# Performance work log

Hardware: AMD Instinct MI355X
Metric: run time of the kernel (lower is better)

Reference implementation:

```python
import jax, jax.numpy as jnp
import numpy as np
from jax import lax

WINDOW = (3, 7, 7)   # per-axis neighborhood kernel size (odd -> centered window)
TILE = (4, 8, 8)     # query tile per axis (must divide T,H,W); FNA-style tiling


def _axis_window(X, k, tq):
    # NATTEN non-causal, stride=1, dilation=1: query i attends keys [s, s+k)
    # with s = clip(i - (k-1)//2, 0, X-k) (centered, clamped at borders).
    starts = np.clip(np.arange(X) - (k - 1) // 2, 0, X - k)          # [X]
    span = tq + k - 1                                                # key block extent per tile
    lead = np.arange(X // tq) * tq                                   # first query of each tile
    base = np.minimum(starts[lead], X - span)                        # [nt] block start (in-bounds)
    gq = lead[:, None] + np.arange(tq)                                # [nt, tq] global query idx
    s = starts[gq][..., None]                                        # [nt, tq, 1]
    j = base[:, None, None] + np.arange(span)                         # [nt, 1, span] global key idx
    valid = (j >= s) & (j < s + k)                                    # [nt, tq, span]
    return base.astype(np.int32), valid


def _na3d(q, k, v, T, H, W):
    B, L, nh, D = q.shape
    assert L == T * H * W
    kT, kH, kW = WINDOW
    qt, qh, qw = TILE
    assert T % qt == 0 and H % qh == 0 and W % qw == 0
    st, sh, sw = qt + kT - 1, qh + kH - 1, qw + kW - 1
    ntT, ntH, ntW = T // qt, H // qh, W // qw
    N = ntT * ntH * ntW
    qvol, svol = qt * qh * qw, st * sh * sw

    baseT, mT = _axis_window(T, kT, qt)
    baseH, mH = _axis_window(H, kH, qh)
    baseW, mW = _axis_window(W, kW, qw)

    # combined per-tile mask: [N, qvol, svol] (static, small)
    mask = (mT[:, None, None, :, None, None, :, None, None]
            & mH[None, :, None, None, :, None, None, :, None]
            & mW[None, None, :, None, None, :, None, None, :])
    mask = jnp.asarray(mask.reshape(N, qvol, svol))

    bT, bH, bW = np.meshgrid(baseT, baseH, baseW, indexing='ij')
    bT = jnp.asarray(bT.ravel()); bH = jnp.asarray(bH.ravel()); bW = jnp.asarray(bW.ravel())

    def to_grid(x):
        return x.reshape(B, T, H, W, nh, D)
    qg, kg, vg = to_grid(q), to_grid(k), to_grid(v)

    # query tiles -> [N, B, qvol, nh, D]
    qt_ = qg.reshape(B, ntT, qt, ntH, qh, ntW, qw, nh, D)
    qt_ = qt_.transpose(1, 3, 5, 0, 2, 4, 6, 7, 8).reshape(N, B, qvol, nh, D)

    # key/value halo blocks per tile -> [N, B, svol, nh, D]
    def slice_blk(arr, t0, h0, w0):
        return lax.dynamic_slice(arr, (0, t0, h0, w0, 0, 0), (B, st, sh, sw, nh, D))
    kblk = jax.vmap(slice_blk, in_axes=(None, 0, 0, 0))(kg, bT, bH, bW).reshape(N, B, svol, nh, D)
    vblk = jax.vmap(slice_blk, in_axes=(None, 0, 0, 0))(vg, bT, bH, bW).reshape(N, B, svol, nh, D)

    scale = D ** -0.5
    scores = jnp.einsum('nbqhd,nbkhd->nbhqk', qt_, kblk) * scale
    scores = jnp.where(mask[:, None, None], scores, -jnp.inf)
    attn = jax.nn.softmax(scores, axis=-1)
    out = jnp.einsum('nbhqk,nbkhd->nbhqd', attn, vblk)

    # scatter tiles back to [B, L, nh, D]
    out = out.reshape(ntT, ntH, ntW, B, nh, qt, qh, qw, D)
    out = out.transpose(3, 0, 5, 1, 6, 2, 7, 4, 8).reshape(B, L, nh, D)
    return out


def setup_inputs() -> dict:
    key = jax.random.key(0)
    k1, k2, k3 = jax.random.split(key, 3)
    B, nh, D = 1, 8, 128
    T, H, W = 16, 32, 32
    L = T * H * W
    q = jax.random.normal(k1, (B, L, nh, D), jnp.float32)
    kk = jax.random.normal(k2, (B, L, nh, D), jnp.float32)
    v = jax.random.normal(k3, (B, L, nh, D), jnp.float32)
    return {"q": q, "k": kk, "v": v, "video_t": T, "video_h": H, "video_w": W}


def reference(q, k, v, video_t, video_h, video_w):
    return _na3d(q, k, v, video_t, video_h, video_w)
```

## Files before the change

kernel.cpp:

```cpp
#include <hip/hip_runtime.h>


typedef _Float16 f16;
typedef _Float16 half8 __attribute__((ext_vector_type(8)));
typedef float floatx4 __attribute__((ext_vector_type(4)));

namespace {

constexpr int T = 16, H = 32, W = 32, NH = 8, D = 128;
constexpr int QT = 2, QH = 4, QW = 8;
constexpr float SCALE = 0.088388347648318447f;

__device__ __forceinline__ int SLOT(int tile, int lr) {
  return tile * 69 + (lr >> 4) * 17 + (lr & 15);
}

__device__ __forceinline__ size_t goff(int tt, int hh, int ww, int head) {
  return ((size_t)((tt * H + hh) * W + ww) * NH + head) * D;
}

__global__ __launch_bounds__(256) void na3d_mfma(
    const float* __restrict__ qp, const float* __restrict__ kp,
    const float* __restrict__ vp, float* __restrict__ op) {
  __shared__ alignas(16) f16 qbuf[16 * 69 * 8];
  __shared__ alignas(16) f16 kvbuf[24 * 69 * 8];
  __shared__ alignas(16) float st[80 * 65];
  __shared__ alignas(16) f16 pbuf[12 * 69 * 8];
  __shared__ alignas(16) float red[4 * 64];
  __shared__ alignas(16) float mnew[64];
  __shared__ alignas(16) float alphas[64];

  int bid = blockIdx.x;
  const int wb = bid & 3;  bid >>= 2;
  const int hb = bid & 7;  bid >>= 3;
  const int tb = bid & 7;  bid >>= 3;
  const int head = bid;

  const int t0 = tb * QT;
  const int h0 = hb * QH, w0 = wb * QW;
  const int bT = min(max(t0 - 1, 0), T - 4);
  const int bH = min(max(h0 - 3, 0), H - 10);
  const int bW = min(max(w0 - 3, 0), W - 14);

  const int tid = threadIdx.x;
  const int wave = tid >> 6, lane = tid & 63;
  const int quad = lane >> 4, ln = lane & 15;

  for (int s = tid; s < 1024; s += 256) {
    const int q = s >> 4, dg = s & 15;
    const size_t off =
        goff(t0 + (q >> 5), h0 + ((q >> 3) & 3), w0 + (q & 7), head) + dg * 8;
    const float4 x0 = *(const float4*)(qp + off);
    const float4 x1 = *(const float4*)(qp + off + 4);
    half8 hv;
    hv[0] = (f16)(x0.x * SCALE); hv[1] = (f16)(x0.y * SCALE);
    hv[2] = (f16)(x0.z * SCALE); hv[3] = (f16)(x0.w * SCALE);
    hv[4] = (f16)(x1.x * SCALE); hv[5] = (f16)(x1.y * SCALE);
    hv[6] = (f16)(x1.z * SCALE); hv[7] = (f16)(x1.w * SCALE);
    const int mt = q >> 4, m = q & 15, ks = dg >> 2, qd = dg & 3;
    *(half8*)&qbuf[SLOT(mt * 4 + ks, qd * 16 + m) * 8] = hv;
  }

  floatx4 oacc[8] = {{0.f, 0.f, 0.f, 0.f}, {0.f, 0.f, 0.f, 0.f},
                     {0.f, 0.f, 0.f, 0.f}, {0.f, 0.f, 0.f, 0.f},
                     {0.f, 0.f, 0.f, 0.f}, {0.f, 0.f, 0.f, 0.f},
                     {0.f, 0.f, 0.f, 0.f}, {0.f, 0.f, 0.f, 0.f}};

  float m_run = -1e30f, l_run = 0.f;

  const int sq = tid & 63, sp = tid >> 6;
  const int aT = min(max(t0 + (sq >> 5) - 1, 0), T - 3) - bT;
  const int aH = min(max(h0 + ((sq >> 3) & 3) - 3, 0), H - 7) - bH;
  const int aW = min(max(w0 + (sq & 7) - 3, 0), W - 7) - bW;

  for (int c = 0; c < 8; ++c) {
    const int dt = c >> 1, hh = c & 1;
    const int tt = bT + dt;
    const int kh0 = bH + hh * 5;
    const bool tOK = (dt >= aT) && (dt < aT + 3);

    __syncthreads();
    for (int s = tid; s < 1120; s += 256) {
      const int kk = s >> 4, dg = s & 15;
      const int khl = kk / 14, kw = kk - khl * 14;
      const size_t off = goff(tt, kh0 + khl, bW + kw, head) + dg * 8;
      const float4 x0 = *(const float4*)(kp + off);
      const float4 x1 = *(const float4*)(kp + off + 4);
      half8 hv;
      hv[0] = (f16)x0.x; hv[1] = (f16)x0.y; hv[2] = (f16)x0.z; hv[3] = (f16)x0.w;
      hv[4] = (f16)x1.x; hv[5] = (f16)x1.y; hv[6] = (f16)x1.z; hv[7] = (f16)x1.w;
      const int nt = kk >> 4, n = kk & 15, ks = dg >> 2, qd = dg & 3;
      *(half8*)&kvbuf[SLOT(nt * 4 + ks, qd * 16 + n) * 8] = hv;
    }
    __syncthreads();

    for (int tile = wave; tile < 20; tile += 4) {
      const int mt = tile / 5, nt = tile - mt * 5;
      floatx4 acc = {0.f, 0.f, 0.f, 0.f};
#pragma unroll
      for (int ks = 0; ks < 4; ++ks) {
        const half8 a = *(const half8*)&qbuf[SLOT(mt * 4 + ks, lane) * 8];
        const half8 b = *(const half8*)&kvbuf[SLOT(nt * 4 + ks, lane) * 8];
        acc = __builtin_amdgcn_mfma_f32_16x16x32_f16(a, b, acc, 0, 0, 0);
      }
      float* dst = &st[(nt * 16 + ln) * 65 + mt * 16 + quad * 4];
      dst[0] = acc[0]; dst[1] = acc[1]; dst[2] = acc[2]; dst[3] = acc[3];
    }
    __syncthreads();

    float pm = -1e30f;
    if (tOK) {
#pragma unroll
      for (int i = 0; i < 18; ++i) {
        const int kk = sp * 18 + i;
        if (kk < 70) {
          const int khl = kk / 14, kw = kk - khl * 14;
          const int kha = hh * 5 + khl;
          if (kha >= aH && kha < aH + 7 && kw >= aW && kw < aW + 7)
            pm = fmaxf(pm, st[kk * 65 + sq]);
        }
      }
    }
    red[sp * 64 + sq] = pm;
    __syncthreads();
    if (tid < 64) {
      float mc = red[tid];
#pragma unroll
      for (int p = 1; p < 4; ++p) mc = fmaxf(mc, red[p * 64 + tid]);
      const float mN = fmaxf(m_run, mc);
      const float a = __expf(m_run - mN);
      m_run = mN; l_run *= a;
      mnew[tid] = mN; alphas[tid] = a;
    }
    __syncthreads();

    {
      const float mq = mnew[sq];
      float ps = 0.f;
      const int mt = sq >> 4, m = sq & 15;
#pragma unroll
      for (int g = 0; g < 3; ++g) {
        const int b = sp * 3 + g;
        const int kst = b >> 2, qd = b & 3;
        half8 pv8;
#pragma unroll
        for (int j = 0; j < 8; ++j) {
          const int kk = b * 8 + j;
          float e = 0.f;
          if (tOK && kk < 70) {
            const int khl = kk / 14, kw = kk - khl * 14;
            const int kha = hh * 5 + khl;
            if (kha >= aH && kha < aH + 7 && kw >= aW && kw < aW + 7) {
              e = __expf(st[kk * 65 + sq] - mq);
              ps += e;
            }
          }
          pv8[j] = (f16)e;
        }
        *(half8*)&pbuf[SLOT(mt * 3 + kst, qd * 16 + m) * 8] = pv8;
      }
      red[sp * 64 + sq] = ps;
    }

    for (int s = tid; s < 1536; s += 256) {
      const int kk = s >> 4, dg = s & 15;
      float xs[8] = {0.f, 0.f, 0.f, 0.f, 0.f, 0.f, 0.f, 0.f};
      if (kk < 70) {
        const int khl = kk / 14, kw = kk - khl * 14;
        const size_t off = goff(tt, kh0 + khl, bW + kw, head) + dg * 8;
        const float4 x0 = *(const float4*)(vp + off);
        const float4 x1 = *(const float4*)(vp + off + 4);
        xs[0] = x0.x; xs[1] = x0.y; xs[2] = x0.z; xs[3] = x0.w;
        xs[4] = x1.x; xs[5] = x1.y; xs[6] = x1.z; xs[7] = x1.w;
      }
      const int kst = kk >> 5, qd = (kk >> 3) & 3, j = kk & 7;
      const int d0 = dg * 8;
#pragma unroll
      for (int u = 0; u < 8; ++u) {
        const int d = d0 + u;
        kvbuf[SLOT((d >> 4) * 3 + kst, qd * 16 + (d & 15)) * 8 + j] =
            (f16)xs[u];
      }
    }
    __syncthreads();

    if (tid < 64) {
      float s2 = 0.f;
#pragma unroll
      for (int p = 0; p < 4; ++p) s2 += red[p * 64 + tid];
      l_run += s2;
    }

    const floatx4 af = *(const floatx4*)&alphas[wave * 16 + quad * 4];
#pragma unroll
    for (int u = 0; u < 8; ++u) oacc[u] *= af;
#pragma unroll
    for (int ks = 0; ks < 3; ++ks) {
      const half8 a = *(const half8*)&pbuf[SLOT(wave * 3 + ks, lane) * 8];
#pragma unroll
      for (int u = 0; u < 8; ++u) {
        const half8 b = *(const half8*)&kvbuf[SLOT(u * 3 + ks, lane) * 8];
        oacc[u] = __builtin_amdgcn_mfma_f32_16x16x32_f16(a, b, oacc[u], 0, 0, 0);
      }
    }
  }

  __syncthreads();
  if (tid < 64) mnew[tid] = 1.f / l_run;
  __syncthreads();
  const floatx4 lf = *(const floatx4*)&mnew[wave * 16 + quad * 4];
#pragma unroll
  for (int r = 0; r < 4; ++r) {
    const int q = wave * 16 + quad * 4 + r;
    const size_t off =
        goff(t0 + (q >> 5), h0 + ((q >> 3) & 3), w0 + (q & 7), head);
#pragma unroll
    for (int u = 0; u < 8; ++u)
      op[off + u * 16 + ln] = oacc[u][r] * lf[r];
  }
}

}

extern "C" void kernel_launch(void* const* d_in, const int* in_sizes, int n_in,
                              void* d_out, int out_size, void* d_ws,
                              size_t ws_size, hipStream_t stream) {
  const float* q = (const float*)d_in[0];
  const float* k = (const float*)d_in[1];
  const float* v = (const float*)d_in[2];
  float* out = (float*)d_out;
  const int nblocks = NH * (T / QT) * (H / QH) * (W / QW);
  na3d_mfma<<<dim3(nblocks), dim3(256), 0, stream>>>(q, k, v, out);
}
```

Before: 528.5 us.

## Keep Q in registers, compute S^T per wave, prefetch K, softmax via shuffles

The kernel now holds the scaled Q fragments in registers and computes the transposed score tile per wave with MFMA. Each wave's 16 queries stay in its accumulators, so the shared-memory score buffer, the reduction arrays and several block barriers go away, and the running max and sum are reduced with cross-lane shuffles. K for the next chunk is prefetched into registers during softmax, and V loads are issued early, with pairs of key rows packed as half2 into shared memory. Custom barriers, a cheaper divide-by-14 and a launch bound of 3 blocks per CU are also added. The cost is much higher register pressure, which may force spills, and more complex indexing.

```diff
diff --git a/kernel.cpp b/kernel.cpp
--- a/kernel.cpp
+++ b/kernel.cpp
@@ -3,7 +3,15 @@
 
 typedef _Float16 f16;
 typedef _Float16 half8 __attribute__((ext_vector_type(8)));
+typedef _Float16 half4 __attribute__((ext_vector_type(4)));
+typedef _Float16 half2 __attribute__((ext_vector_type(2)));
 typedef float floatx4 __attribute__((ext_vector_type(4)));
+typedef float floatv4 __attribute__((ext_vector_type(4)));
+
+#define CFENCE() asm volatile("" ::: "memory")
+#define BAR_PLAIN() do { CFENCE(); __builtin_amdgcn_s_barrier(); CFENCE(); } while (0)
+#define BAR_LDSW() do { asm volatile("s_waitcnt lgkmcnt(0)" ::: "memory"); \
+                        __builtin_amdgcn_s_barrier(); CFENCE(); } while (0)
 
 namespace {
 
@@ -19,16 +27,13 @@
   return ((size_t)((tt * H + hh) * W + ww) * NH + head) * D;
 }
 
-__global__ __launch_bounds__(256) void na3d_mfma(
+__device__ __forceinline__ int div14(int x) { return (x * 586) >> 13; }
+
+__global__ __launch_bounds__(256, 3) void na3d_mfma(
     const float* __restrict__ qp, const float* __restrict__ kp,
     const float* __restrict__ vp, float* __restrict__ op) {
-  __shared__ alignas(16) f16 qbuf[16 * 69 * 8];
   __shared__ alignas(16) f16 kvbuf[24 * 69 * 8];
-  __shared__ alignas(16) float st[80 * 65];
   __shared__ alignas(16) f16 pbuf[12 * 69 * 8];
-  __shared__ alignas(16) float red[4 * 64];
-  __shared__ alignas(16) float mnew[64];
-  __shared__ alignas(16) float alphas[64];
 
   int bid = blockIdx.x;
   const int wb = bid & 3;  bid >>= 2;
@@ -45,153 +50,201 @@
   const int tid = threadIdx.x;
   const int wave = tid >> 6, lane = tid & 63;
   const int quad = lane >> 4, ln = lane & 15;
-
-  for (int s = tid; s < 1024; s += 256) {
-    const int q = s >> 4, dg = s & 15;
-    const size_t off =
-        goff(t0 + (q >> 5), h0 + ((q >> 3) & 3), w0 + (q & 7), head) + dg * 8;
-    const float4 x0 = *(const float4*)(qp + off);
-    const float4 x1 = *(const float4*)(qp + off + 4);
-    half8 hv;
-    hv[0] = (f16)(x0.x * SCALE); hv[1] = (f16)(x0.y * SCALE);
-    hv[2] = (f16)(x0.z * SCALE); hv[3] = (f16)(x0.w * SCALE);
-    hv[4] = (f16)(x1.x * SCALE); hv[5] = (f16)(x1.y * SCALE);
-    hv[6] = (f16)(x1.z * SCALE); hv[7] = (f16)(x1.w * SCALE);
-    const int mt = q >> 4, m = q & 15, ks = dg >> 2, qd = dg & 3;
-    *(half8*)&qbuf[SLOT(mt * 4 + ks, qd * 16 + m) * 8] = hv;
+  const int kbase = quad * 4;
+
+  const int toff = wave >> 1;
+  const int hoff = (wave & 1) * 2 + (ln >> 3);
+  const int woff = ln & 7;
+  const int aT = min(max(t0 + toff - 1, 0), T - 3) - bT;
+  const int aH = min(max(h0 + hoff - 3, 0), H - 7) - bH;
+  const int aW = min(max(w0 + woff - 3, 0), W - 7) - bW;
+
+  half8 qreg[4];
+  {
+    const size_t row = goff(t0 + toff, h0 + hoff, w0 + woff, head);
+#pragma unroll
+    for (int ks = 0; ks < 4; ++ks) {
+      const int d0 = ks * 32 + quad * 8;
+      const floatv4 x0 = *(const floatv4*)(qp + row + d0);
+      const floatv4 x1 = *(const floatv4*)(qp + row + d0 + 4);
+      half8 hv;
+      hv[0] = (f16)(x0[0] * SCALE); hv[1] = (f16)(x0[1] * SCALE);
+      hv[2] = (f16)(x0[2] * SCALE); hv[3] = (f16)(x0[3] * SCALE);
+      hv[4] = (f16)(x1[0] * SCALE); hv[5] = (f16)(x1[1] * SCALE);
+      hv[6] = (f16)(x1[2] * SCALE); hv[7] = (f16)(x1[3] * SCALE);
+      qreg[ks] = hv;
+    }
+  }
+
+  if (quad >= 2) {
+    *(floatx4*)&pbuf[SLOT(wave * 3 + 2, lane) * 8] = (floatx4){0.f, 0.f, 0.f, 0.f};
   }
 
   floatx4 oacc[8] = {{0.f, 0.f, 0.f, 0.f}, {0.f, 0.f, 0.f, 0.f},
                      {0.f, 0.f, 0.f, 0.f}, {0.f, 0.f, 0.f, 0.f},
                      {0.f, 0.f, 0.f, 0.f}, {0.f, 0.f, 0.f, 0.f},
                      {0.f, 0.f, 0.f, 0.f}, {0.f, 0.f, 0.f, 0.f}};
-
   float m_run = -1e30f, l_run = 0.f;
 
-  const int sq = tid & 63, sp = tid >> 6;
-  const int aT = min(max(t0 + (sq >> 5) - 1, 0), T - 3) - bT;
-  const int aH = min(max(h0 + ((sq >> 3) & 3) - 3, 0), H - 7) - bH;
-  const int aW = min(max(w0 + (sq & 7) - 3, 0), W - 7) - bW;
+  floatv4 kreg[5][2];
+  floatv4 vreg[3][4];
+
+  {
+    const int tt = bT, kh0 = bH;
+#pragma unroll
+    for (int it = 0; it < 5; ++it) {
+      const int s = tid + it * 256;
+      if (s < 1120) {
+        const int kk = s >> 4, dg = s & 15;
+        const int khl = div14(kk), kw = kk - khl * 14;
+        const size_t off = goff(tt, kh0 + khl, bW + kw, head) + dg * 8;
+        kreg[it][0] = *(const floatv4*)(kp + off);
+        kreg[it][1] = *(const floatv4*)(kp + off + 4);
+      }
+    }
+  }
 
   for (int c = 0; c < 8; ++c) {
-    const int dt = c >> 1, hh = c & 1;
+    const int dt = c >> 1;
     const int tt = bT + dt;
-    const int kh0 = bH + hh * 5;
+    const int kh0 = bH + (c & 1) * 5;
+    const int hh5 = (c & 1) * 5;
     const bool tOK = (dt >= aT) && (dt < aT + 3);
 
-    __syncthreads();
-    for (int s = tid; s < 1120; s += 256) {
-      const int kk = s >> 4, dg = s & 15;
-      const int khl = kk / 14, kw = kk - khl * 14;
-      const size_t off = goff(tt, kh0 + khl, bW + kw, head) + dg * 8;
-      const float4 x0 = *(const float4*)(kp + off);
-      const float4 x1 = *(const float4*)(kp + off + 4);
-      half8 hv;
-      hv[0] = (f16)x0.x; hv[1] = (f16)x0.y; hv[2] = (f16)x0.z; hv[3] = (f16)x0.w;
-      hv[4] = (f16)x1.x; hv[5] = (f16)x1.y; hv[6] = (f16)x1.z; hv[7] = (f16)x1.w;
-      const int nt = kk >> 4, n = kk & 15, ks = dg >> 2, qd = dg & 3;
-      *(half8*)&kvbuf[SLOT(nt * 4 + ks, qd * 16 + n) * 8] = hv;
-    }
-    __syncthreads();
-
-    for (int tile = wave; tile < 20; tile += 4) {
-      const int mt = tile / 5, nt = tile - mt * 5;
-      floatx4 acc = {0.f, 0.f, 0.f, 0.f};
+    BAR_PLAIN();
+
+#pragma unroll
+    for (int it = 0; it < 5; ++it) {
+      const int s = tid + it * 256;
+      if (s < 1120) {
+        const int kk = s >> 4, dg = s & 15;
+        const floatv4 a0 = kreg[it][0], a1 = kreg[it][1];
+        half8 hv;
+        hv[0] = (f16)a0[0]; hv[1] = (f16)a0[1];
+        hv[2] = (f16)a0[2]; hv[3] = (f16)a0[3];
+        hv[4] = (f16)a1[0]; hv[5] = (f16)a1[1];
+        hv[6] = (f16)a1[2]; hv[7] = (f16)a1[3];
+        *(half8*)&kvbuf[SLOT((kk >> 4) * 4 + (dg >> 2),
+                             (dg & 3) * 16 + (kk & 15)) * 8] = hv;
+      }
+    }
+
+#pragma unroll
+    for (int it = 0; it < 3; ++it) {
+      const int s = tid + it * 256;
+      const int p = s >> 4, dg = s & 15;
+      const int kk0 = p * 2;
+      if (kk0 < 70) {
+        const int khl = div14(kk0), kw = kk0 - khl * 14;
+        const size_t off = goff(tt, kh0 + khl, bW + kw, head) + dg * 8;
+        vreg[it][0] = *(const floatv4*)(vp + off);
+        vreg[it][1] = *(const floatv4*)(vp + off + 4);
+        vreg[it][2] = *(const floatv4*)(vp + off + 1024);
+        vreg[it][3] = *(const floatv4*)(vp + off + 1028);
+      } else {
+        vreg[it][0] = (floatv4){0.f, 0.f, 0.f, 0.f};
+        vreg[it][1] = (floatv4){0.f, 0.f, 0.f, 0.f};
+        vreg[it][2] = (floatv4){0.f, 0.f, 0.f, 0.f};
+        vreg[it][3] = (floatv4){0.f, 0.f, 0.f, 0.f};
+      }
+    }
+
+    BAR_LDSW();
+
+    floatx4 acc1[5] = {{0.f, 0.f, 0.f, 0.f}, {0.f, 0.f, 0.f, 0.f},
+                       {0.f, 0.f, 0.f, 0.f}, {0.f, 0.f, 0.f, 0.f},
+                       {0.f, 0.f, 0.f, 0.f}};
+#pragma unroll
+    for (int kt = 0; kt < 5; ++kt) {
 #pragma unroll
       for (int ks = 0; ks < 4; ++ks) {
-        const half8 a = *(const half8*)&qbuf[SLOT(mt * 4 + ks, lane) * 8];
-        const half8 b = *(const half8*)&kvbuf[SLOT(nt * 4 + ks, lane) * 8];
-        acc = __builtin_amdgcn_mfma_f32_16x16x32_f16(a, b, acc, 0, 0, 0);
-      }
-      float* dst = &st[(nt * 16 + ln) * 65 + mt * 16 + quad * 4];
-      dst[0] = acc[0]; dst[1] = acc[1]; dst[2] = acc[2]; dst[3] = acc[3];
-    }
-    __syncthreads();
+        const half8 a = *(const half8*)&kvbuf[SLOT(kt * 4 + ks, lane) * 8];
+        acc1[kt] =
+            __builtin_amdgcn_mfma_f32_16x16x32_f16(a, qreg[ks], acc1[kt], 0, 0, 0);
+      }
+    }
+
+    BAR_PLAIN();
+
+#pragma unroll
+    for (int it = 0; it < 3; ++it) {
+      const int s = tid + it * 256;
+      const int p = s >> 4, dg = s & 15;
+      const int kk0 = p * 2;
+      const int kst = kk0 >> 5, qd = (kk0 >> 3) & 3, j0 = kk0 & 7;
+      const int tbase = (dg >> 1) * 3 + kst;
+      const int lrb = qd * 16 + (dg & 1) * 8;
+#pragma unroll
+      for (int u = 0; u < 8; ++u) {
+        half2 h;
+        h[0] = (f16)vreg[it][u >> 2][u & 3];
+        h[1] = (f16)vreg[it][2 + (u >> 2)][u & 3];
+        *(half2*)&kvbuf[SLOT(tbase, lrb + u) * 8 + j0] = h;
+      }
+    }
+
+    if (c < 7) {
+      const int cc = c + 1;
+      const int ttn = bT + (cc >> 1);
+      const int kh0n = bH + (cc & 1) * 5;
+#pragma unroll
+      for (int it = 0; it < 5; ++it) {
+        const int s = tid + it * 256;
+        if (s < 1120) {
+          const int kk = s >> 4, dg = s & 15;
+          const int khl = div14(kk), kw = kk - khl * 14;
+          const size_t off = goff(ttn, kh0n + khl, bW + kw, head) + dg * 8;
+          kreg[it][0] = *(const floatv4*)(kp + off);
+          kreg[it][1] = *(const floatv4*)(kp + off + 4);
+        }
+      }
+    }
 
     float pm = -1e30f;
-    if (tOK) {
-#pragma unroll
-      for (int i = 0; i < 18; ++i) {
-        const int kk = sp * 18 + i;
-        if (kk < 70) {
-          const int khl = kk / 14, kw = kk - khl * 14;
-          const int kha = hh * 5 + khl;
-          if (kha >= aH && kha < aH + 7 && kw >= aW && kw < aW + 7)
-            pm = fmaxf(pm, st[kk * 65 + sq]);
-        }
-      }
-    }
-    red[sp * 64 + sq] = pm;
-    __syncthreads();
-    if (tid < 64) {
-      float mc = red[tid];
-#pragma unroll
-      for (int p = 1; p < 4; ++p) mc = fmaxf(mc, red[p * 64 + tid]);
-      const float mN = fmaxf(m_run, mc);
-      const float a = __expf(m_run - mN);
-      m_run = mN; l_run *= a;
-      mnew[tid] = mN; alphas[tid] = a;
-    }
-    __syncthreads();
-
-    {
-      const float mq = mnew[sq];
-      float ps = 0.f;
-      const int mt = sq >> 4, m = sq & 15;
-#pragma unroll
-      for (int g = 0; g < 3; ++g) {
-        const int b = sp * 3 + g;
-        const int kst = b >> 2, qd = b & 3;
-        half8 pv8;
-#pragma unroll
-        for (int j = 0; j < 8; ++j) {
-          const int kk = b * 8 + j;
-          float e = 0.f;
-          if (tOK && kk < 70) {
-            const int khl = kk / 14, kw = kk - khl * 14;
-            const int kha = hh * 5 + khl;
-            if (kha >= aH && kha < aH + 7 && kw >= aW && kw < aW + 7) {
-              e = __expf(st[kk * 65 + sq] - mq);
-              ps += e;
-            }
-          }
-          pv8[j] = (f16)e;
-        }
-        *(half8*)&pbuf[SLOT(mt * 3 + kst, qd * 16 + m) * 8] = pv8;
-      }
-      red[sp * 64 + sq] = ps;
-    }
-
-    for (int s = tid; s < 1536; s += 256) {
-      const int kk = s >> 4, dg = s & 15;
-      float xs[8] = {0.f, 0.f, 0.f, 0.f, 0.f, 0.f, 0.f, 0.f};
-      if (kk < 70) {
-        const int khl = kk / 14, kw = kk - khl * 14;
-        const size_t off = goff(tt, kh0 + khl, bW + kw, head) + dg * 8;
-        const float4 x0 = *(const float4*)(vp + off);
-        const float4 x1 = *(const float4*)(vp + off + 4);
-        xs[0] = x0.x; xs[1] = x0.y; xs[2] = x0.z; xs[3] = x0.w;
-        xs[4] = x1.x; xs[5] = x1.y; xs[6] = x1.z; xs[7] = x1.w;
-      }
-      const int kst = kk >> 5, qd = (kk >> 3) & 3, j = kk & 7;
-      const int d0 = dg * 8;
-#pragma unroll
-      for (int u = 0; u < 8; ++u) {
-        const int d = d0 + u;
-        kvbuf[SLOT((d >> 4) * 3 + kst, qd * 16 + (d & 15)) * 8 + j] =
-            (f16)xs[u];
-      }
-    }
-    __syncthreads();
-
-    if (tid < 64) {
-      float s2 = 0.f;
-#pragma unroll
-      for (int p = 0; p < 4; ++p) s2 += red[p * 64 + tid];
-      l_run += s2;
-    }
-
-    const floatx4 af = *(const floatx4*)&alphas[wave * 16 + quad * 4];
+#pragma unroll
+    for (int kt = 0; kt < 5; ++kt) {
+#pragma unroll
+      for (int r = 0; r < 4; ++r) {
+        const int kk = kt * 16 + kbase + r;
+        const int khl = div14(kk), kw = kk - khl * 14;
+        const int kha = hh5 + khl;
+        const bool ok = tOK && (kk < 70) && ((unsigned)(kha - aH) < 7u) &&
+                        ((unsigned)(kw - aW) < 7u);
+        const float sv = ok ? acc1[kt][r] : -INFINITY;
+        acc1[kt][r] = sv;
+        pm = fmaxf(pm, sv);
+      }
+    }
+    pm = fmaxf(pm, __shfl_xor(pm, 16));
+    pm = fmaxf(pm, __shfl_xor(pm, 32));
+    const float mN = fmaxf(m_run, pm);
+    const float alpha = __expf(m_run - mN);
+    m_run = mN;
+
+    float ps = 0.f;
+#pragma unroll
+    for (int kt = 0; kt < 5; ++kt) {
+      half4 h;
+#pragma unroll
+      for (int r = 0; r < 4; ++r) {
+        const float e = __expf(acc1[kt][r] - mN);
+        ps += e;
+        h[r] = (f16)e;
+      }
+      *(half4*)&pbuf[SLOT(wave * 3 + (kt >> 1),
+                          ((kt & 1) * 2 + (quad >> 1)) * 16 + ln) * 8 +
+                     (quad & 1) * 4] = h;
+    }
+    ps += __shfl_xor(ps, 16);
+    ps += __shfl_xor(ps, 32);
+    l_run = l_run * alpha + ps;
+
+    BAR_LDSW();
+    __builtin_amdgcn_sched_barrier(0);
+
+    floatx4 af;
+#pragma unroll
+    for (int r = 0; r < 4; ++r) af[r] = __shfl(alpha, kbase + r);
 #pragma unroll
     for (int u = 0; u < 8; ++u) oacc[u] *= af;
 #pragma unroll
@@ -205,10 +258,10 @@
     }
   }
 
-  __syncthreads();
-  if (tid < 64) mnew[tid] = 1.f / l_run;
-  __syncthreads();
-  const floatx4 lf = *(const floatx4*)&mnew[wave * 16 + quad * 4];
+  const float linv = 1.f / l_run;
+  floatx4 lf;
+#pragma unroll
+  for (int r = 0; r < 4; ++r) lf[r] = __shfl(linv, kbase + r);
 #pragma unroll
   for (int r = 0; r < 4; ++r) {
     const int q = wave * 16 + quad * 4 + r;
```

Result: faster. 496.5 us (-6.1%).
